# Kernel optimization log

Measured on AMD Instinct MI355X. Metric: run time of the kernel, lower is better.

## Reference

```python
import jax, jax.numpy as jnp
import numpy as np

H, C = 3, 64  # heads, per-head channels
NEG_SLOPE = 0.2

def setup_inputs() -> dict:
    key = jax.random.key(0)
    ks = jax.random.split(key, 8)
    B, N, D, E = 2, 50000, 128, 800000
    h = jax.random.normal(ks[0], (B, N, D), dtype=jnp.float32)
    edge_index = jax.random.randint(ks[1], (2, E), 0, N, dtype=jnp.int64)
    s = 1.0 / np.sqrt(D)
    W = jax.random.normal(ks[2], (D, H * C), dtype=jnp.float32) * s
    a_src = jax.random.normal(ks[3], (H, C), dtype=jnp.float32) * (1.0 / np.sqrt(C))
    a_dst = jax.random.normal(ks[4], (H, C), dtype=jnp.float32) * (1.0 / np.sqrt(C))
    bias = jnp.zeros((H * C,), dtype=jnp.float32)
    Wo = jax.random.normal(ks[5], (H * C, 1), dtype=jnp.float32) * (1.0 / np.sqrt(H * C))
    bo = jnp.zeros((1,), dtype=jnp.float32)
    return {"h": h, "edge_index": edge_index, "W": W, "a_src": a_src,
            "a_dst": a_dst, "bias": bias, "Wo": Wo, "bo": bo}

def _gat_single(h_b, src, dst, N, W, a_src, a_dst, bias):
    # h_b: [N, D] -> x: [N, H, C]
    x = (h_b @ W).reshape(-1, H, C)
    alpha_s = jnp.einsum('nhc,hc->nh', x, a_src)  # [N, H]
    alpha_d = jnp.einsum('nhc,hc->nh', x, a_dst)  # [N, H]
    e = alpha_s[src] + alpha_d[dst]               # [E', H]
    e = jnp.where(e > 0, e, NEG_SLOPE * e)        # leaky_relu(0.2)
    # segment softmax over edges grouped by destination node
    emax = jax.ops.segment_max(e, dst, num_segments=N)          # [N, H]
    p = jnp.exp(e - emax[dst])
    denom = jax.ops.segment_sum(p, dst, num_segments=N)         # [N, H]
    att = p / (denom[dst] + 1e-16)                               # [E', H]
    out = jax.ops.segment_sum(att[:, :, None] * x[src], dst, num_segments=N)  # [N,H,C]
    return out.reshape(-1, H * C) + bias

def reference(h, edge_index, W, a_src, a_dst, bias, Wo, bo):
    B, N, D = h.shape
    # PyG GATConv default: add self loops
    loops = jnp.arange(N, dtype=edge_index.dtype)
    src = jnp.concatenate([edge_index[0], loops])
    dst = jnp.concatenate([edge_index[1], loops])
    gat = jax.vmap(lambda hb: _gat_single(hb, src, dst, N, W, a_src, a_dst, bias))(h)
    gat = jax.nn.elu(gat)            # [B, N, H*C]; dropout inactive (eval)
    logits = gat @ Wo + bo           # [B, N, 1]
    return logits
```

## Files before the change

### kernel.cpp

```cpp
#include <hip/hip_runtime.h>
#include <hip/hip_bf16.h>
#include <math.h>

typedef __hip_bfloat16 bf16;
typedef __attribute__((ext_vector_type(8))) short short8;
typedef __attribute__((ext_vector_type(4))) short short4v;
typedef __attribute__((ext_vector_type(4))) float f32x4;

#define HC 192
#define DIN 128
#define NEG_SLOPE 0.2f
#define GN 4
#define CAP 56
#define GROWS 128

static inline int cdiv(int a, int b){ return (a + b - 1) / b; }

__device__ inline short f2bf(float f){
  __hip_bfloat16 b = __float2bfloat16(f);
  return __builtin_bit_cast(short, b);
}
__device__ inline float loadf(const void* p, size_t i, int fm){
  return fm ? __bfloat162float(((const bf16*)p)[i]) : ((const float*)p)[i];
}
__device__ inline int eload(const void* p, long long i, int em){
  return em ? (int)(((const long long*)p)[i]) : ((const int*)p)[i];
}

__device__ inline int detect_fm(const unsigned* __restrict__ hw){
  unsigned w = hw[threadIdx.x & 63];
  unsigned expo = (w >> 7) & 0xFF;
  unsigned long long m = __ballot(expo >= 100 && expo <= 135);
  return __popcll(m) > 32;
}
__device__ inline int detect_em(const unsigned* __restrict__ ew){
  unsigned long long m = __ballot(ew[2*(threadIdx.x & 63) + 1] != 0);
  return __popcll(m) < 32;
}

__global__ void k_repack(const void* __restrict__ W, const void* __restrict__ a_src,
    const void* __restrict__ a_dst, const void* __restrict__ bias,
    const void* __restrict__ Wo, const void* __restrict__ bo,
    const unsigned* __restrict__ hw, bf16* __restrict__ Wt,
    float* __restrict__ asf, float* __restrict__ adf, float* __restrict__ biasf,
    float* __restrict__ Wof, float* __restrict__ bof,
    int* __restrict__ counts, int N){
  int fm = detect_fm(hw);
  int idx = blockIdx.x * 256 + threadIdx.x;
  for (int i = idx; i < N; i += 96 * 256) counts[i] = 0;
  if (idx < DIN * HC){
    int d = idx / HC, j = idx - d * HC;
    Wt[j * DIN + d] = __float2bfloat16(loadf(W, idx, fm));
  }
  if (idx < HC){
    asf[idx]   = loadf(a_src, idx, fm);
    adf[idx]   = loadf(a_dst, idx, fm);
    biasf[idx] = loadf(bias, idx, fm);
    Wof[idx]   = loadf(Wo, idx, fm);
  }
  if (idx == 0) bof[0] = loadf(bo, 0, fm);
}

__global__ void k_bucket(const void* __restrict__ ei, int E, int N,
    int* __restrict__ counts, unsigned* __restrict__ srcs){
  int em = detect_em((const unsigned*)ei);
  int idx = blockIdx.x * 256 + threadIdx.x;
  if (idx >= E + N) return;
  int s, d;
  if (idx < E){
    s = eload(ei, idx, em);
    d = eload(ei, (long long)E + idx, em);
  } else { s = d = idx - E; }
  if ((unsigned)d >= (unsigned)N) return;
  if ((unsigned)s >= (unsigned)N) s = 0;
  int slot = atomicAdd(&counts[d], 1);
  if (slot >= CAP) return;
  srcs[(size_t)d * CAP + slot] = (unsigned)s;
}

__global__ __launch_bounds__(512) void k_gemm(const void* __restrict__ h,
    const bf16* __restrict__ Wt, bf16* __restrict__ x,
    const float* __restrict__ asf, const float* __restrict__ adf,
    float* __restrict__ asp, float* __restrict__ adp, int M, int N){
  int fm   = detect_fm((const unsigned*)h);
  int tid  = threadIdx.x;
  int w    = tid >> 6;
  int lane = tid & 63;
  int r16  = lane & 15;
  int quad = lane >> 4;
  __shared__ short ldsW[HC * 136];
  for (int c = tid; c < HC * 16; c += 512){
    int row = c >> 4, kg = c & 15;
    *(short8*)&ldsW[row * 136 + kg * 8] = *(const short8*)(Wt + row * DIN + kg * 8);
  }
  __syncthreads();

  int row  = blockIdx.x * GROWS + w * 16 + r16;
  int lrow = min(row, M - 1);
  f32x4 acc[12];
  #pragma unroll
  for (int i = 0; i < 12; i++) acc[i] = (f32x4){0.f,0.f,0.f,0.f};
  size_t hbase = (size_t)lrow * DIN + quad * 8;
  #pragma unroll
  for (int kb = 0; kb < 4; kb++){
    short8 bh;
    if (fm == 0){
      const float* hf = (const float*)h + hbase + kb * 32;
      float4 a = *(const float4*)hf;
      float4 b = *(const float4*)(hf + 4);
      bh[0]=f2bf(a.x); bh[1]=f2bf(a.y); bh[2]=f2bf(a.z); bh[3]=f2bf(a.w);
      bh[4]=f2bf(b.x); bh[5]=f2bf(b.y); bh[6]=f2bf(b.z); bh[7]=f2bf(b.w);
    } else {
      bh = *(const short8*)((const bf16*)h + hbase + kb * 32);
    }
    #pragma unroll
    for (int nt = 0; nt < 12; nt++){
      short8 aw = *(const short8*)&ldsW[(nt*16 + r16) * 136 + kb * 32 + quad * 8];
      acc[nt] = __builtin_amdgcn_mfma_f32_16x16x32_bf16(aw, bh, acc[nt], 0,0,0);
    }
  }
  if (row < M){
    int bb    = row >= N;
    int nodeR = row - bb * N;
    bf16* xr  = x + ((size_t)nodeR * 2 + bb) * HC;
    #pragma unroll
    for (int nt = 0; nt < 12; nt++){
      short4v pk = { f2bf(acc[nt][0]), f2bf(acc[nt][1]),
                     f2bf(acc[nt][2]), f2bf(acc[nt][3]) };
      *(short4v*)(xr + nt*16 + quad*4) = pk;
    }
  }
  float vs[3] = {0.f,0.f,0.f}, vd[3] = {0.f,0.f,0.f};
  #pragma unroll
  for (int nt = 0; nt < 12; nt++){
    int hh = nt >> 2;
    f32x4 a4 = *(const f32x4*)(asf + nt*16 + quad*4);
    f32x4 d4 = *(const f32x4*)(adf + nt*16 + quad*4);
    vs[hh] += acc[nt][0]*a4[0] + acc[nt][1]*a4[1] + acc[nt][2]*a4[2] + acc[nt][3]*a4[3];
    vd[hh] += acc[nt][0]*d4[0] + acc[nt][1]*d4[1] + acc[nt][2]*d4[2] + acc[nt][3]*d4[3];
  }
  #pragma unroll
  for (int hh = 0; hh < 3; hh++){
    float v1 = vs[hh], v2 = vd[hh];
    v1 += __shfl_down(v1, 32);  v1 += __shfl_down(v1, 16);
    v2 += __shfl_down(v2, 32);  v2 += __shfl_down(v2, 16);
    if (lane < 16 && row < M){
      int b = row >= N;
      int node = row - b * N;
      asp[(size_t)node*8 + b*3 + hh] = v1;
      adp[(size_t)node*8 + b*3 + hh] = v2;
    }
  }
}

__global__ __launch_bounds__(192) void k_gat(const bf16* __restrict__ x,
    const unsigned* __restrict__ srcs, const int* __restrict__ cnt,
    const float* __restrict__ asp, const float* __restrict__ adp,
    const float* __restrict__ biasf, const float* __restrict__ Wof,
    const float* __restrict__ bof, float* __restrict__ out, int N){
  int blk  = blockIdx.x;
  int t    = threadIdx.x;
  int node = t / 48;
  int u    = t - node * 48;
  int b    = u >= 24;
  int c8   = u - b * 24;
  int hh   = c8 >> 3;
  __shared__ int      cs[GN];
  __shared__ unsigned ldsS[GN * CAP];
  __shared__ float    red[192];
  if (t < GN) cs[t] = min(cnt[GN*blk + t], CAP);
  __syncthreads();
  for (int j = t; j < GN * CAP; j += 192){
    int nd = j / CAP, sl = j - nd * CAP;
    if (sl < cs[nd]) ldsS[j] = srcs[(size_t)(GN*blk + nd) * CAP + sl];
  }
  __syncthreads();
  int mycnt = cs[node];
  int d     = GN*blk + node;
  int pidx  = b*3 + hh;
  float adv = adp[(size_t)d * 8 + pidx];
  const ushort* xb = (const ushort*)x + (size_t)b * HC + c8 * 8;
  float acc[8];
  #pragma unroll
  for (int k = 0; k < 8; k++) acc[k] = 0.f;
  float den = 0.f;
  int rbase = node * CAP;
  #pragma unroll 8
  for (int i = 0; i < mycnt; i++){
    int s   = (int)ldsS[rbase + i];
    float e = asp[(size_t)s * 8 + pidx] + adv;
    e = e > 0.f ? e : NEG_SLOPE * e;
    float p = __expf(e);
    uint4 q = *(const uint4*)(xb + (size_t)s * (2 * HC));
    den += p;
    acc[0] = fmaf(p, __uint_as_float(q.x << 16),         acc[0]);
    acc[1] = fmaf(p, __uint_as_float(q.x & 0xffff0000u), acc[1]);
    acc[2] = fmaf(p, __uint_as_float(q.y << 16),         acc[2]);
    acc[3] = fmaf(p, __uint_as_float(q.y & 0xffff0000u), acc[3]);
    acc[4] = fmaf(p, __uint_as_float(q.z << 16),         acc[4]);
    acc[5] = fmaf(p, __uint_as_float(q.z & 0xffff0000u), acc[5]);
    acc[6] = fmaf(p, __uint_as_float(q.w << 16),         acc[6]);
    acc[7] = fmaf(p, __uint_as_float(q.w & 0xffff0000u), acc[7]);
  }
  float inv = 1.f / (den + 1e-16f);
  float4 bi0 = ((const float4*)biasf)[c8*2], bi1 = ((const float4*)biasf)[c8*2+1];
  float4 w0  = ((const float4*)Wof)[c8*2],  w1  = ((const float4*)Wof)[c8*2+1];
  float r = 0.f;
  {
    float v;
    v = acc[0]*inv + bi0.x; v = v > 0.f ? v : expm1f(v); r += v * w0.x;
    v = acc[1]*inv + bi0.y; v = v > 0.f ? v : expm1f(v); r += v * w0.y;
    v = acc[2]*inv + bi0.z; v = v > 0.f ? v : expm1f(v); r += v * w0.z;
    v = acc[3]*inv + bi0.w; v = v > 0.f ? v : expm1f(v); r += v * w0.w;
    v = acc[4]*inv + bi1.x; v = v > 0.f ? v : expm1f(v); r += v * w1.x;
    v = acc[5]*inv + bi1.y; v = v > 0.f ? v : expm1f(v); r += v * w1.y;
    v = acc[6]*inv + bi1.z; v = v > 0.f ? v : expm1f(v); r += v * w1.z;
    v = acc[7]*inv + bi1.w; v = v > 0.f ? v : expm1f(v); r += v * w1.w;
  }
  red[t] = r;
  __syncthreads();
  if (t < 64){
    int g = t >> 3, l = t & 7;
    float v = red[g*24 + l] + red[g*24 + 8 + l] + red[g*24 + 16 + l];
    v += __shfl_down(v, 4, 8);
    v += __shfl_down(v, 2, 8);
    v += __shfl_down(v, 1, 8);
    if (l == 0){
      int nd = GN*blk + (g >> 1);
      int bb = g & 1;
      out[(size_t)bb * N + nd] = v + bof[0];
    }
  }
}

extern "C" void kernel_launch(void* const* d_in, const int* in_sizes, int n_in,
                              void* d_out, int out_size, void* d_ws, size_t ws_size,
                              hipStream_t stream){
  const void* h     = d_in[0];
  const void* ei    = d_in[1];
  const void* W     = d_in[2];
  const void* a_src = d_in[3];
  const void* a_dst = d_in[4];
  const void* bias  = d_in[5];
  const void* Wo    = d_in[6];
  const void* bo    = d_in[7];
  float* out = (float*)d_out;

  const int M    = in_sizes[0] / DIN;
  const int N    = M / 2;
  const int E    = in_sizes[1] / 2;
  const int Etot = E + N;

  char* ws = (char*)d_ws;
  size_t off = 0;
  auto alloc = [&](size_t bytes) -> void* {
    void* p = ws + off;
    off = (off + bytes + 511) & ~(size_t)511;
    return p;
  };
  bf16*     x      = (bf16*)    alloc((size_t)M * HC * sizeof(bf16));
  float*    asp    = (float*)   alloc((size_t)N * 8 * sizeof(float));
  float*    adp    = (float*)   alloc((size_t)N * 8 * sizeof(float));
  int*      counts = (int*)     alloc((size_t)N * sizeof(int));
  unsigned* srcs   = (unsigned*)alloc((size_t)N * CAP * sizeof(unsigned));
  bf16*     Wt     = (bf16*)    alloc((size_t)DIN * HC * sizeof(bf16));
  float*    asf    = (float*)   alloc(HC * sizeof(float));
  float*    adf    = (float*)   alloc(HC * sizeof(float));
  float*    biasf  = (float*)   alloc(HC * sizeof(float));
  float*    Wof    = (float*)   alloc(HC * sizeof(float));
  float*    bof    = (float*)   alloc(16 * sizeof(float));
  (void)ws_size; (void)n_in; (void)out_size;

  k_repack<<<96, 256, 0, stream>>>(W, a_src, a_dst, bias, Wo, bo,
      (const unsigned*)h, Wt, asf, adf, biasf, Wof, bof, counts, N);
  k_bucket<<<cdiv(Etot, 256), 256, 0, stream>>>(ei, E, N, counts, srcs);
  k_gemm<<<cdiv(M, GROWS), 512, 0, stream>>>(h, Wt, x, asf, adf, asp, adp, M, N);
  k_gat<<<N / GN, 192, 0, stream>>>(x, srcs, counts, asp, adp, biasf, Wof, bof, out, N);
}
```

Baseline: 280.9 us.

## Merge edge bucketing into GEMM launch and precompute attention weights in LDS

The independent edge-bucketing work is folded into the GEMM kernel as extra blocks, so bucketing and the projection GEMM run concurrently in one launch instead of two serialized ones. Bucketing blocks still reserve the GEMM's large LDS array, which may limit their occupancy. Separately, the GAT kernel now computes all six per-edge exp(leaky_relu) weights once per edge into LDS, instead of each of 48 threads per node reloading asp and recomputing exp. This adds a barrier and more LDS use per block.

```diff
diff --git a/kernel.cpp b/kernel.cpp
--- a/kernel.cpp
+++ b/kernel.cpp
@@ -61,41 +61,44 @@
   if (idx == 0) bof[0] = loadf(bo, 0, fm);
 }
 
-__global__ void k_bucket(const void* __restrict__ ei, int E, int N,
-    int* __restrict__ counts, unsigned* __restrict__ srcs){
-  int em = detect_em((const unsigned*)ei);
-  int idx = blockIdx.x * 256 + threadIdx.x;
-  if (idx >= E + N) return;
-  int s, d;
-  if (idx < E){
-    s = eload(ei, idx, em);
-    d = eload(ei, (long long)E + idx, em);
-  } else { s = d = idx - E; }
-  if ((unsigned)d >= (unsigned)N) return;
-  if ((unsigned)s >= (unsigned)N) s = 0;
-  int slot = atomicAdd(&counts[d], 1);
-  if (slot >= CAP) return;
-  srcs[(size_t)d * CAP + slot] = (unsigned)s;
-}
-
-__global__ __launch_bounds__(512) void k_gemm(const void* __restrict__ h,
+__global__ __launch_bounds__(512) void k_fused(const void* __restrict__ h,
     const bf16* __restrict__ Wt, bf16* __restrict__ x,
     const float* __restrict__ asf, const float* __restrict__ adf,
-    float* __restrict__ asp, float* __restrict__ adp, int M, int N){
+    float* __restrict__ asp, float* __restrict__ adp,
+    const void* __restrict__ ei, int* __restrict__ counts,
+    unsigned* __restrict__ srcs, int M, int N, int E, int NBG){
+  __shared__ short ldsW[HC * 136];
+
+  if ((int)blockIdx.x >= NBG){
+    int em = detect_em((const unsigned*)ei);
+    int idx = ((int)blockIdx.x - NBG) * 512 + (int)threadIdx.x;
+    if (idx >= E + N) return;
+    int s, d;
+    if (idx < E){
+      s = eload(ei, idx, em);
+      d = eload(ei, (long long)E + idx, em);
+    } else { s = d = idx - E; }
+    if ((unsigned)d >= (unsigned)N) return;
+    if ((unsigned)s >= (unsigned)N) s = 0;
+    int slot = atomicAdd(&counts[d], 1);
+    if (slot >= CAP) return;
+    srcs[(size_t)d * CAP + slot] = (unsigned)s;
+    return;
+  }
+
   int fm   = detect_fm((const unsigned*)h);
   int tid  = threadIdx.x;
   int w    = tid >> 6;
   int lane = tid & 63;
   int r16  = lane & 15;
   int quad = lane >> 4;
-  __shared__ short ldsW[HC * 136];
   for (int c = tid; c < HC * 16; c += 512){
     int row = c >> 4, kg = c & 15;
     *(short8*)&ldsW[row * 136 + kg * 8] = *(const short8*)(Wt + row * DIN + kg * 8);
   }
   __syncthreads();
 
-  int row  = blockIdx.x * GROWS + w * 16 + r16;
+  int row  = (int)blockIdx.x * GROWS + w * 16 + r16;
   int lrow = min(row, M - 1);
   f32x4 acc[12];
   #pragma unroll
@@ -166,19 +169,41 @@
   int c8   = u - b * 24;
   int hh   = c8 >> 3;
   __shared__ int      cs[GN];
+  __shared__ float    adl[GN * 6];
   __shared__ unsigned ldsS[GN * CAP];
+  __shared__ float    ldsP[GN * CAP * 6];
   __shared__ float    red[192];
   if (t < GN) cs[t] = min(cnt[GN*blk + t], CAP);
+  if (t < GN * 6){
+    int nd = t / 6, k = t - nd * 6;
+    adl[t] = adp[(size_t)(GN*blk + nd) * 8 + k];
+  }
   __syncthreads();
   for (int j = t; j < GN * CAP; j += 192){
     int nd = j / CAP, sl = j - nd * CAP;
     if (sl < cs[nd]) ldsS[j] = srcs[(size_t)(GN*blk + nd) * CAP + sl];
   }
   __syncthreads();
+  for (int j = t; j < GN * CAP; j += 192){
+    int nd = j / CAP, sl = j - nd * CAP;
+    if (sl < cs[nd]){
+      int s = (int)ldsS[j];
+      float4 A0 = *(const float4*)(asp + (size_t)s * 8);
+      float4 A1 = *(const float4*)(asp + (size_t)s * 8 + 4);
+      float e0 = A0.x + adl[nd*6+0], e1 = A0.y + adl[nd*6+1];
+      float e2 = A0.z + adl[nd*6+2], e3 = A0.w + adl[nd*6+3];
+      float e4 = A1.x + adl[nd*6+4], e5 = A1.y + adl[nd*6+5];
+      e0 = e0 > 0.f ? e0 : NEG_SLOPE*e0;  e1 = e1 > 0.f ? e1 : NEG_SLOPE*e1;
+      e2 = e2 > 0.f ? e2 : NEG_SLOPE*e2;  e3 = e3 > 0.f ? e3 : NEG_SLOPE*e3;
+      e4 = e4 > 0.f ? e4 : NEG_SLOPE*e4;  e5 = e5 > 0.f ? e5 : NEG_SLOPE*e5;
+      ldsP[j*6 + 0] = __expf(e0);  ldsP[j*6 + 1] = __expf(e1);
+      ldsP[j*6 + 2] = __expf(e2);  ldsP[j*6 + 3] = __expf(e3);
+      ldsP[j*6 + 4] = __expf(e4);  ldsP[j*6 + 5] = __expf(e5);
+    }
+  }
+  __syncthreads();
   int mycnt = cs[node];
-  int d     = GN*blk + node;
   int pidx  = b*3 + hh;
-  float adv = adp[(size_t)d * 8 + pidx];
   const ushort* xb = (const ushort*)x + (size_t)b * HC + c8 * 8;
   float acc[8];
   #pragma unroll
@@ -187,10 +212,9 @@
   int rbase = node * CAP;
   #pragma unroll 8
   for (int i = 0; i < mycnt; i++){
-    int s   = (int)ldsS[rbase + i];
-    float e = asp[(size_t)s * 8 + pidx] + adv;
-    e = e > 0.f ? e : NEG_SLOPE * e;
-    float p = __expf(e);
+    int rec = rbase + i;
+    float p = ldsP[rec*6 + pidx];
+    int s   = (int)ldsS[rec];
     uint4 q = *(const uint4*)(xb + (size_t)s * (2 * HC));
     den += p;
     acc[0] = fmaf(p, __uint_as_float(q.x << 16),         acc[0]);
@@ -271,9 +295,13 @@
   float*    bof    = (float*)   alloc(16 * sizeof(float));
   (void)ws_size; (void)n_in; (void)out_size;
 
+  const int NBG = cdiv(M, GROWS);
+  const int NBB = cdiv(Etot, 512);
+
   k_repack<<<96, 256, 0, stream>>>(W, a_src, a_dst, bias, Wo, bo,
       (const unsigned*)h, Wt, asf, adf, biasf, Wof, bof, counts, N);
-  k_bucket<<<cdiv(Etot, 256), 256, 0, stream>>>(ei, E, N, counts, srcs);
-  k_gemm<<<cdiv(M, GROWS), 512, 0, stream>>>(h, Wt, x, asf, adf, asp, adp, M, N);
-  k_gat<<<N / GN, 192, 0, stream>>>(x, srcs, counts, asp, adp, biasf, Wof, bof, out, N);
-}
+  k_fused<<<NBG + NBB, 512, 0, stream>>>(h, Wt, x, asf, adf, asp, adp,
+      ei, counts, srcs, M, N, E, NBG);
+  k_gat<<<N / GN, 192, 0, stream>>>(x, srcs, counts, asp, adp,
+      biasf, Wof, bof, out, N);
+}
```

Result: faster. 265.3 us, median of 2 (-5.6%).
